# Kernel tuning notes

Measured on AMD Instinct MI355X. Metric: run time of the kernel, lower is better.

The kernel has to match this reference:

```python
import jax, jax.numpy as jnp
import numpy as np

B, S, E, H = 2, 2048, 1024, 16
D = E // H  # head_dim = 64
EPS = 1e-6


def _angle_decay():
    # angle: 1/10000**linspace(0,1,D//2), each value repeated twice (interleaved)
    a = 1.0 / (10000.0 ** jnp.linspace(0.0, 1.0, D // 2))
    angle = jnp.repeat(a, 2)  # [D]
    decay = jnp.log(1.0 - 2.0 ** (-5.0 - jnp.arange(H, dtype=jnp.float32)))  # [H]
    return angle, decay


def _rel_pos(slen):
    angle, decay = _angle_decay()
    idx = jnp.arange(slen, dtype=jnp.float32)
    sin = jnp.sin(idx[:, None] * angle[None, :])  # [S, D]
    cos = jnp.cos(idx[:, None] * angle[None, :])  # [S, D]
    diff = idx[:, None] - idx[None, :]            # [S, S]
    tril = diff >= 0
    masked = jnp.where(tril, diff, jnp.inf)
    mask = jnp.exp(masked * decay[:, None, None])  # [H, S, S]; exp(-inf)=0 on upper tri
    mask = jnp.nan_to_num(mask)
    mask = mask / jnp.sqrt(jnp.sum(mask, axis=-1, keepdims=True))
    return sin, cos, mask


def _rotate_every_two(x):
    x1 = x[..., ::2]
    x2 = x[..., 1::2]
    return jnp.stack((-x2, x1), axis=-1).reshape(x.shape)


def _theta_shift(x, sin, cos):
    # x: [B, H, S, D]; sin/cos: [S, D] broadcast over B,H
    return x * cos + _rotate_every_two(x) * sin


def setup_inputs() -> dict:
    key = jax.random.key(0)
    ks = jax.random.split(key, 5)
    scale = 1.0 / np.sqrt(E)
    return {
        "x": jax.random.normal(ks[0], (B, S, E), dtype=jnp.float32),
        "Wq": jax.random.normal(ks[1], (E, E), dtype=jnp.float32) * scale,
        "Wk": jax.random.normal(ks[2], (E, E), dtype=jnp.float32) * scale,
        "Wv": jax.random.normal(ks[3], (E, E), dtype=jnp.float32) * scale,
        "Wg": jax.random.normal(ks[4], (E, E), dtype=jnp.float32) * scale,
    }


def reference(x, Wq, Wk, Wv, Wg):
    bsz, tgt_len, _ = x.shape
    sin, cos, mask = _rel_pos(tgt_len)
    scaling = E ** (-0.5)

    q = x @ Wq
    k = (x @ Wk) * scaling
    v = x @ Wv
    g = x @ Wg

    q = q.reshape(bsz, tgt_len, H, D).transpose(0, 2, 1, 3)  # [B,H,S,D]
    k = k.reshape(bsz, tgt_len, H, D).transpose(0, 2, 1, 3)
    vr = v.reshape(bsz, tgt_len, H, D).transpose(0, 2, 1, 3)

    qr = _theta_shift(q, sin, cos)
    kr = _theta_shift(k, sin, cos)

    qk = jnp.einsum("bhqd,bhkd->bhqk", qr, kr) * mask[None]
    denom = jax.lax.stop_gradient(
        jnp.clip(jnp.sum(jnp.abs(qk), axis=-1, keepdims=True), 1.0, 5e4)
    )
    out = jnp.einsum("bhqk,bhkd->bhqd", qk / denom, vr)
    out = out.transpose(0, 2, 1, 3)  # [B,S,H,D]

    # RMSNorm over head_dim (no affine)
    out = out * jax.lax.rsqrt(jnp.mean(out * out, axis=-1, keepdims=True) + EPS)
    out = out.reshape(bsz, tgt_len, E)
    return jax.nn.silu(g) * out
```

## Files before the change

kernel.cpp:

```cpp
#include <hip/hip_runtime.h>

typedef unsigned short u16;
typedef unsigned int u32;
typedef __attribute__((ext_vector_type(8))) __bf16 bf16x8;
typedef __attribute__((ext_vector_type(4))) float f32x4;

#define B_SZ   2
#define S_LEN  2048
#define E_DIM  1024
#define NHEAD  16
#define HD     64
#define KDIM   1024

__device__ __forceinline__ float bf2f(u16 u){
  union { u32 i; float f; } c; c.i = ((u32)u) << 16; return c.f;
}
__device__ __forceinline__ u16 f2bf(float f){
  union { float f; u32 i; } c; c.f = f;
  return (u16)((c.i + 0x7FFFu + ((c.i >> 16) & 1u)) >> 16);
}
__device__ __forceinline__ u32 cvtpk_bf16(float lo, float hi){
  u32 r; asm("v_cvt_pk_bf16_f32 %0, %1, %2" : "=v"(r) : "v"(lo), "v"(hi)); return r;
}
__device__ __forceinline__ void gl2lds16(const void* g, void* l){
  __builtin_amdgcn_global_load_lds((const __attribute__((address_space(1))) void*)g,
                                   (__attribute__((address_space(3))) void*)l, 16, 0, 0);
}

__global__ __launch_bounds__(256) void prep_kernel(const float* __restrict__ x,
                                                   const float* __restrict__ Wq, const float* __restrict__ Wk,
                                                   const float* __restrict__ Wv, const float* __restrict__ Wg,
                                                   u16* __restrict__ xb, u16* __restrict__ WT){
  __shared__ u16 tile[64][66];
  int z = blockIdx.z;
  int t = threadIdx.x;
  if (z < 4){
    const float* Ws[4] = {Wq, Wk, Wv, Wg};
    const float* W = Ws[z];
    int n0 = blockIdx.x * 64, k0 = blockIdx.y * 64;
    int r = t >> 2, cg = (t & 3) * 16;
    const float* src = W + (size_t)(k0 + r) * E_DIM + n0 + cg;
    float f[16];
    #pragma unroll
    for (int c = 0; c < 4; c++) *(float4*)&f[c * 4] = *(const float4*)&src[c * 4];
    #pragma unroll
    for (int i = 0; i < 16; i++) tile[r][cg + i] = f2bf(f[i]);
    __syncthreads();
    u16 ov[16];
    #pragma unroll
    for (int i = 0; i < 16; i++) ov[i] = tile[cg + i][r];
    int n7 = r & 7, cb = cg >> 3;
    u16* dst = WT + (size_t)(z * E_DIM + n0 + r) * KDIM + k0;
    *(uint4*)&dst[(cb ^ n7) * 8]       = *(uint4*)&ov[0];
    *(uint4*)&dst[((cb + 1) ^ n7) * 8] = *(uint4*)&ov[8];
  } else {
    int blk = (z - 4) * 256 + blockIdx.y * 16 + blockIdx.x;
    size_t flat = ((size_t)blk * 256 + t) * 16;
    int m7 = (int)((flat >> 10) & 7);
    int cb = (int)((flat >> 3) & 7);
    size_t tl = flat & ~(size_t)63;
    float f[16];
    #pragma unroll
    for (int c = 0; c < 4; c++) *(float4*)&f[c * 4] = *(const float4*)&x[flat + c * 4];
    u16 o[16];
    #pragma unroll
    for (int i = 0; i < 16; i++) o[i] = f2bf(f[i]);
    *(uint4*)&xb[tl + ((cb ^ m7) * 8)]       = *(uint4*)&o[0];
    *(uint4*)&xb[tl + (((cb + 1) ^ m7) * 8)] = *(uint4*)&o[8];
  }
}

__global__ __launch_bounds__(512, 2) void gemm_kernel(const u16* __restrict__ A, const u16* __restrict__ Bt,
                                                      u16* __restrict__ qr, u16* __restrict__ kr,
                                                      u16* __restrict__ vt, u16* __restrict__ gc){
  __shared__ __align__(16) u16 SH[65536];
  int m0 = blockIdx.y * 256, n0 = blockIdx.x * 256;
  int t = threadIdx.x;
  int wave = t >> 6, lane = t & 63;
  int l15 = lane & 15, quad = lane >> 4, h8 = lane & 7;
  int wm = wave >> 2, wn = wave & 3;

  f32x4 acc[8][4];
  #pragma unroll
  for (int i = 0; i < 8; i++)
    #pragma unroll
    for (int j = 0; j < 4; j++) acc[i][j] = (f32x4){0.f, 0.f, 0.f, 0.f};

  auto Aoff = [&](int buf, int half) -> int { return (buf * 2 + half) * 8192; };
  auto Boff = [&](int buf, int half) -> int { return 32768 + (buf * 2 + half) * 8192; };

  auto stA = [&](int buf, int half, int kt){
    const u16* src = A + (size_t)(m0 + half * 128) * KDIM + kt * 64;
    #pragma unroll
    for (int c = 0; c < 2; c++){
      int L = c * 512 + t;
      gl2lds16(src + (size_t)(L >> 3) * KDIM + (L & 7) * 8, &SH[Aoff(buf, half) + L * 8]);
    }
  };
  auto stB = [&](int buf, int half, int kt){
    const u16* src = Bt + (size_t)(n0 + half * 128) * KDIM + kt * 64;
    #pragma unroll
    for (int c = 0; c < 2; c++){
      int L = c * 512 + t;
      gl2lds16(src + (size_t)(L >> 3) * KDIM + (L & 7) * 8, &SH[Boff(buf, half) + L * 8]);
    }
  };
  auto ldA = [&](int buf, int i, int ks) -> bf16x8 {
    int r = i * 16 + l15;
    return *(const bf16x8*)&SH[Aoff(buf, wm) + r * 64 + (((ks * 4 + quad) ^ h8) * 8)];
  };
  auto ldB = [&](int buf, int j, int ks) -> bf16x8 {
    int c = (wn & 1) * 64 + j * 16 + l15;
    return *(const bf16x8*)&SH[Boff(buf, wn >> 1) + c * 64 + (((ks * 4 + quad) ^ h8) * 8)];
  };

  stA(0, 0, 0); stB(0, 0, 0); stA(0, 1, 0); stB(0, 1, 0);
  asm volatile("s_waitcnt vmcnt(0)" ::: "memory");
  __builtin_amdgcn_s_barrier();

  bf16x8 a[4][2];
  bf16x8 bA[2][2];
  bf16x8 bB[2][2];

  for (int t2 = 0; t2 < 8; ++t2){
    int kt0 = 2 * t2;
    bool more = (t2 < 7);

    #pragma unroll
    for (int half = 0; half < 2; ++half){
      int buf = half;
      bool stg = (buf == 0) || more;
      {
        #pragma unroll
        for (int i = 0; i < 4; i++){ a[i][0] = ldA(buf, i, 0); a[i][1] = ldA(buf, i, 1); }
        #pragma unroll
        for (int j = 0; j < 2; j++){ bA[j][0] = ldB(buf, j, 0); bA[j][1] = ldB(buf, j, 1); }
        if (buf == 0){ stA(1, 0, kt0 + 1); stB(1, 0, kt0 + 1); }
        else if (more){ stA(0, 0, kt0 + 2); stB(0, 0, kt0 + 2); }
        __builtin_amdgcn_sched_barrier(0);
        __builtin_amdgcn_s_barrier();
        asm volatile("s_waitcnt lgkmcnt(0)" ::: "memory");
        __builtin_amdgcn_sched_barrier(0);
        __builtin_amdgcn_s_setprio(1);
        #pragma unroll
        for (int i = 0; i < 4; i++)
          #pragma unroll
          for (int j = 0; j < 2; j++){
            acc[i][j] = __builtin_amdgcn_mfma_f32_16x16x32_bf16(a[i][0], bA[j][0], acc[i][j], 0, 0, 0);
            acc[i][j] = __builtin_amdgcn_mfma_f32_16x16x32_bf16(a[i][1], bA[j][1], acc[i][j], 0, 0, 0);
          }
        __builtin_amdgcn_s_setprio(0);
        __builtin_amdgcn_sched_barrier(0);
        __builtin_amdgcn_s_barrier();
      }
      {
        #pragma unroll
        for (int j = 0; j < 2; j++){ bB[j][0] = ldB(buf, j + 2, 0); bB[j][1] = ldB(buf, j + 2, 1); }
        if (buf == 0){ stA(1, 1, kt0 + 1); stB(1, 1, kt0 + 1); }
        else if (more){ stA(0, 1, kt0 + 2); stB(0, 1, kt0 + 2); }
        __builtin_amdgcn_sched_barrier(0);
        __builtin_amdgcn_s_barrier();
        asm volatile("s_waitcnt lgkmcnt(0)" ::: "memory");
        __builtin_amdgcn_sched_barrier(0);
        __builtin_amdgcn_s_setprio(1);
        #pragma unroll
        for (int i = 0; i < 4; i++)
          #pragma unroll
          for (int j = 0; j < 2; j++){
            acc[i][j + 2] = __builtin_amdgcn_mfma_f32_16x16x32_bf16(a[i][0], bB[j][0], acc[i][j + 2], 0, 0, 0);
            acc[i][j + 2] = __builtin_amdgcn_mfma_f32_16x16x32_bf16(a[i][1], bB[j][1], acc[i][j + 2], 0, 0, 0);
          }
        __builtin_amdgcn_s_setprio(0);
        __builtin_amdgcn_sched_barrier(0);
        __builtin_amdgcn_s_barrier();
      }
      {
        #pragma unroll
        for (int i = 0; i < 4; i++){ a[i][0] = ldA(buf, i + 4, 0); a[i][1] = ldA(buf, i + 4, 1); }
        __builtin_amdgcn_sched_barrier(0);
        __builtin_amdgcn_s_barrier();
        asm volatile("s_waitcnt lgkmcnt(0)" ::: "memory");
        __builtin_amdgcn_sched_barrier(0);
        __builtin_amdgcn_s_setprio(1);
        #pragma unroll
        for (int i = 0; i < 4; i++)
          #pragma unroll
          for (int j = 0; j < 2; j++){
            acc[i + 4][j + 2] = __builtin_amdgcn_mfma_f32_16x16x32_bf16(a[i][0], bB[j][0], acc[i + 4][j + 2], 0, 0, 0);
            acc[i + 4][j + 2] = __builtin_amdgcn_mfma_f32_16x16x32_bf16(a[i][1], bB[j][1], acc[i + 4][j + 2], 0, 0, 0);
          }
        #pragma unroll
        for (int i = 0; i < 4; i++)
          #pragma unroll
          for (int j = 0; j < 2; j++){
            acc[i + 4][j] = __builtin_amdgcn_mfma_f32_16x16x32_bf16(a[i][0], bA[j][0], acc[i + 4][j], 0, 0, 0);
            acc[i + 4][j] = __builtin_amdgcn_mfma_f32_16x16x32_bf16(a[i][1], bA[j][1], acc[i + 4][j], 0, 0, 0);
          }
        __builtin_amdgcn_s_setprio(0);
        __builtin_amdgcn_sched_barrier(0);
        if (stg) { asm volatile("s_waitcnt vmcnt(0)" ::: "memory"); }
        __builtin_amdgcn_s_barrier();
      }
    }
  }

  __syncthreads();
  u16* epi = SH + wave * 8192;
  int zone = n0 >> 10;
  int n0l = n0 & 1023;
  int hh = (n0l >> 6) + wn;
  int b = m0 >> 11;
  int s0f = (m0 & 2047) + wm * 128;

  if (zone == 2){
    #pragma unroll
    for (int j = 0; j < 4; j++){
      int d = j * 16 + l15;
      #pragma unroll
      for (int i = 0; i < 8; i++){
        int cs0 = i * 2 + (quad >> 1);
        u16 pk[4];
        #pragma unroll
        for (int r = 0; r < 4; r++) pk[r] = f2bf(acc[i][j][r]);
        *(uint2*)&epi[d * 128 + ((cs0 ^ (d & 7)) * 8) + (quad & 1) * 4] = *(uint2*)pk;
      }
    }
    __syncthreads();
    int dl = lane >> 4, cl = lane & 15;
    size_t vbase = (size_t)((b << 4) + hh) * HD * S_LEN;
    #pragma unroll
    for (int it = 0; it < 16; it++){
      int d = it * 4 + dl;
      uint4 v = *(const uint4*)&epi[d * 128 + cl * 8];
      *(uint4*)&vt[vbase + (size_t)d * S_LEN + s0f + cl * 8] = v;
    }
  } else if (zone == 3){
    #pragma unroll
    for (int j = 0; j < 4; j++){
      int c0c = 2 * j + (l15 >> 3), o7 = l15 & 7;
      #pragma unroll
      for (int i = 0; i < 8; i++)
        #pragma unroll
        for (int r = 0; r < 4; r++){
          int row = i * 16 + quad * 4 + r;
          epi[row * 64 + ((c0c ^ (row & 7)) * 8) + o7] = f2bf(acc[i][j][r]);
        }
    }
    __syncthreads();
    int rl = lane >> 3, cl = lane & 7;
    #pragma unroll
    for (int it = 0; it < 16; it++){
      int row = it * 8 + rl;
      uint4 v = *(const uint4*)&epi[row * 64 + ((cl ^ (row & 7)) * 8)];
      *(uint4*)&gc[(size_t)(m0 + wm * 128 + row) * E_DIM + n0l + wn * 64 + cl * 8] = v;
    }
  } else {
    float scale = (zone == 1) ? 0.03125f : 1.0f;
    float sgn = (l15 & 1) ? 1.0f : -1.0f;
    #pragma unroll
    for (int j = 0; j < 4; j++){
      int d = j * 16 + l15;
      int c0c = 2 * j + (l15 >> 3), o7 = l15 & 7;
      float af = exp2f(-(float)(d >> 1) * (13.287712379549449f / 31.0f));
      float cs, sn, ca1, sa1, cb, sb_;
      __sincosf((float)(s0f + quad * 4) * af, &sn, &cs);
      __sincosf(af, &sa1, &ca1);
      __sincosf(13.0f * af, &sb_, &cb);
      #pragma unroll
      for (int i = 0; i < 8; i++)
        #pragma unroll
        for (int r = 0; r < 4; r++){
          int row = i * 16 + quad * 4 + r;
          float vv = acc[i][j][r] * scale;
          float p = __shfl_xor(vv, 1);
          float outv = vv * cs + sgn * p * sn;
          epi[row * 64 + ((c0c ^ (row & 7)) * 8) + o7] = f2bf(outv);
          float nc, ns;
          if (r < 3){ nc = cs * ca1 - sn * sa1; ns = sn * ca1 + cs * sa1; }
          else      { nc = cs * cb  - sn * sb_; ns = sn * cb  + cs * sb_; }
          cs = nc; sn = ns;
        }
    }
    __syncthreads();
    int rl = lane >> 3, cl = lane & 7;
    size_t qkbase = (size_t)((b << 4) + hh) * S_LEN + s0f;
    u16* dst = (zone == 0) ? qr : kr;
    #pragma unroll
    for (int it = 0; it < 16; it++){
      int row = it * 8 + rl;
      int rp = (zone == 0) ? (cl ^ (row & 7)) : cl;
      uint4 v = *(const uint4*)&epi[row * 64 + rp * 8];
      *(uint4*)&dst[(qkbase + row) * HD + cl * 8] = v;
    }
  }
}

__global__ __launch_bounds__(256, 3) void retention_kernel(const u16* __restrict__ qr, const u16* __restrict__ kr,
                                                           const u16* __restrict__ vt,
                                                           u16* __restrict__ pO, u16* __restrict__ pBa){
  __shared__ __align__(16) u16 Ks[2][4096];
  __shared__ __align__(16) u16 Vs[2][4096];
  __shared__ __align__(16) u16 Ps[128 * 72];
  int bh = blockIdx.x;
  int qb = 15 - (int)blockIdx.y;
  int z  = blockIdx.z;
  int h = bh & 15;
  int q0 = qb * 128;

  float decay = log1pf(-exp2f(-5.0f - (float)h));
  float negd = -decay;
  float win_f = 11.0f / negd;
  int win_i = (win_f > 2.1e9f) ? 0x7f000000 : (int)win_f;
  int nk = 2 * qb + 2;
  int z_lo = (z * nk) >> 2;
  int z_hi = (((z + 1) * nk) >> 2) - 1;
  int kb_lo = z_lo;
  {
    int jmin = q0 - win_i;
    if (jmin > z_lo * 64){ int wlo = jmin >> 6; kb_lo = wlo > z_lo ? wlo : z_lo; }
  }
  if (kb_lo > z_hi) return;

  int t = threadIdx.x, wave = t >> 6, lane = t & 63;
  int l15 = lane & 15, quad = lane >> 4, h8 = lane & 7;
  float estep = __expf(64.0f * negd);

  int qsE[2], rowb[2];
  #pragma unroll
  for (int e = 0; e < 2; e++){ rowb[e] = wave * 32 + e * 16; qsE[e] = q0 + rowb[e]; }

  bf16x8 qB[2][2];
  #pragma unroll
  for (int e = 0; e < 2; e++){
    size_t qrow = ((size_t)bh * S_LEN + qsE[e] + l15) * HD;
    qB[e][0] = *(const bf16x8*)&qr[qrow + quad * 8];
    qB[e][1] = *(const bf16x8*)&qr[qrow + 32 + quad * 8];
  }

  int k0s = kb_lo * 64;
  float em1d = expm1f(decay);
  float rfE[2]; int iE[2];
  #pragma unroll
  for (int e = 0; e < 2; e++){
    int i = qsE[e] + l15;
    iE[e] = i;
    float rowsum = expm1f((float)(i + 1) * decay) / em1d;
    rfE[e] = __expf((float)(i - k0s) * decay) * rsqrtf(rowsum);
  }
  float e1 = __expf(negd);
  float c16 = __expf(negd * 16.0f);
  float cbr[4];
  cbr[0] = __expf(negd * (float)(quad * 4));
  cbr[1] = cbr[0] * e1; cbr[2] = cbr[1] * e1; cbr[3] = cbr[2] * e1;

  f32x4 o[2][4];
  #pragma unroll
  for (int e = 0; e < 2; e++)
    #pragma unroll
    for (int dt = 0; dt < 4; dt++) o[e][dt] = (f32x4){0.f, 0.f, 0.f, 0.f};
  float babs[2] = {0.f, 0.f};

  const u16* krbh = kr + (size_t)bh * S_LEN * HD;
  const u16* vtbh = vt + (size_t)bh * HD * S_LEN;

  auto stKV = [&](int kb, int slot){
    int k0 = kb * 64;
    #pragma unroll
    for (int c = 0; c < 2; c++){
      int L = c * 256 + t;
      gl2lds16(krbh + (size_t)k0 * HD + L * 8, &Ks[slot][L * 8]);
    }
    #pragma unroll
    for (int c = 0; c < 2; c++){
      int L = c * 256 + t;
      gl2lds16(vtbh + (size_t)(L >> 3) * S_LEN + k0 + (L & 7) * 8, &Vs[slot][L * 8]);
    }
  };

  stKV(kb_lo, 0);
  __syncthreads();
  int cur = 0;
  for (int kb = kb_lo; kb <= z_hi; kb++){
    if (kb < z_hi) stKV(kb + 1, cur ^ 1);

    int k0 = kb * 64;
    const u16* KsC = &Ks[cur][0];
    const u16* VsC = &Vs[cur][0];

    bf16x8 kA0[4], kA1[4];
    #pragma unroll
    for (int ct = 0; ct < 4; ct++){
      int rw = (ct * 16 + l15) * 64;
      kA0[ct] = *(const bf16x8*)&KsC[rw + ((quad ^ h8) * 8)];
      kA1[ct] = *(const bf16x8*)&KsC[rw + (((quad + 4) ^ h8) * 8)];
    }
    #pragma unroll
    for (int e = 0; e < 2; e++){
      int qs = qsE[e];
      if (k0 <= qs + 15 && k0 + 63 >= qs - win_i){
        float rc0 = rfE[e] * cbr[0], rc1 = rfE[e] * cbr[1];
        float rc2 = rfE[e] * cbr[2], rc3 = rfE[e] * cbr[3];
        if (k0 + 64 <= qs){
          #pragma unroll
          for (int ct = 0; ct < 4; ct++){
            f32x4 zacc = (f32x4){0.f, 0.f, 0.f, 0.f};
            zacc = __builtin_amdgcn_mfma_f32_16x16x32_bf16(kA0[ct], qB[e][0], zacc, 0, 0, 0);
            zacc = __builtin_amdgcn_mfma_f32_16x16x32_bf16(kA1[ct], qB[e][1], zacc, 0, 0, 0);
            float p0 = zacc[0] * rc0, p1 = zacc[1] * rc1, p2 = zacc[2] * rc2, p3 = zacc[3] * rc3;
            babs[e] += fabsf(p0); babs[e] += fabsf(p1); babs[e] += fabsf(p2); babs[e] += fabsf(p3);
            u32 lo = cvtpk_bf16(p0, p1), hi = cvtpk_bf16(p2, p3);
            rc0 *= c16; rc1 *= c16; rc2 *= c16; rc3 *= c16;
            *(uint2*)&Ps[(rowb[e] + l15) * 72 + ct * 16 + quad * 4] = make_uint2(lo, hi);
          }
        } else {
          #pragma unroll
          for (int ct = 0; ct < 4; ct++){
            f32x4 zacc = (f32x4){0.f, 0.f, 0.f, 0.f};
            zacc = __builtin_amdgcn_mfma_f32_16x16x32_bf16(kA0[ct], qB[e][0], zacc, 0, 0, 0);
            zacc = __builtin_amdgcn_mfma_f32_16x16x32_bf16(kA1[ct], qB[e][1], zacc, 0, 0, 0);
            int kbase = k0 + ct * 16 + quad * 4;
            float p0 = zacc[0] * rc0, p1 = zacc[1] * rc1, p2 = zacc[2] * rc2, p3 = zacc[3] * rc3;
            if (kbase + 0 > iE[e]) p0 = 0.f;
            if (kbase + 1 > iE[e]) p1 = 0.f;
            if (kbase + 2 > iE[e]) p2 = 0.f;
            if (kbase + 3 > iE[e]) p3 = 0.f;
            babs[e] += fabsf(p0); babs[e] += fabsf(p1); babs[e] += fabsf(p2); babs[e] += fabsf(p3);
            u32 lo = cvtpk_bf16(p0, p1), hi = cvtpk_bf16(p2, p3);
            rc0 *= c16; rc1 *= c16; rc2 *= c16; rc3 *= c16;
            *(uint2*)&Ps[(rowb[e] + l15) * 72 + ct * 16 + quad * 4] = make_uint2(lo, hi);
          }
        }
      }
    }
    #pragma unroll
    for (int e = 0; e < 2; e++){
      int qs = qsE[e];
      if (k0 <= qs + 15 && k0 + 63 >= qs - win_i){
        bf16x8 pB0 = *(const bf16x8*)&Ps[(rowb[e] + l15) * 72 + quad * 8];
        bf16x8 pB1 = *(const bf16x8*)&Ps[(rowb[e] + l15) * 72 + 32 + quad * 8];
        #pragma unroll
        for (int dt = 0; dt < 4; dt++){
          int rw = (dt * 16 + l15) * 64;
          bf16x8 vA0 = *(const bf16x8*)&VsC[rw + ((quad ^ h8) * 8)];
          bf16x8 vA1 = *(const bf16x8*)&VsC[rw + (((quad + 4) ^ h8) * 8)];
          o[e][dt] = __builtin_amdgcn_mfma_f32_16x16x32_bf16(vA0, pB0, o[e][dt], 0, 0, 0);
          o[e][dt] = __builtin_amdgcn_mfma_f32_16x16x32_bf16(vA1, pB1, o[e][dt], 0, 0, 0);
        }
      }
    }
    #pragma unroll
    for (int e = 0; e < 2; e++) rfE[e] *= estep;
    __syncthreads();
    cur ^= 1;
  }

  size_t slot = ((size_t)bh * 16 + qb) * 4 + z;
  u16* po = pO + slot * (4 * 128 * 16);
  #pragma unroll
  for (int e = 0; e < 2; e++){
    float bsum = babs[e];
    bsum += __shfl_xor(bsum, 16);
    bsum += __shfl_xor(bsum, 32);
    if (quad == 0) pBa[slot * 128 + rowb[e] + l15] = f2bf(bsum);
    #pragma unroll
    for (int dt = 0; dt < 4; dt++){
      u16 pk[4];
      #pragma unroll
      for (int r = 0; r < 4; r++) pk[r] = f2bf(o[e][dt][r]);
      *(uint2*)&po[(dt * 128 + rowb[e] + l15) * 16 + quad * 4] = *(uint2*)pk;
    }
  }
}

__global__ __launch_bounds__(128) void combine_kernel(const u16* __restrict__ pO, const u16* __restrict__ pBa,
                                                      const u16* __restrict__ gc, float* __restrict__ out){
  int bh = blockIdx.x, qb = blockIdx.y;
  int b = bh >> 4, h = bh & 15;
  int i = threadIdx.x;
  int s = qb * 128 + i;
  size_t s4 = ((size_t)bh * 16 + qb) * 4;

  float decay = log1pf(-exp2f(-5.0f - (float)h));
  float negd = -decay;
  float win_f = 11.0f / negd;
  int win_i = (win_f > 2.1e9f) ? 0x7f000000 : (int)win_f;
  int nk = 2 * qb + 2;
  int q0 = qb * 128;

  float v[64];
  #pragma unroll
  for (int d = 0; d < 64; d++) v[d] = 0.f;
  float bsum = 0.f;
  #pragma unroll
  for (int z = 0; z < 4; z++){
    int z_lo = (z * nk) >> 2;
    int z_hi = (((z + 1) * nk) >> 2) - 1;
    int kb_lo = z_lo;
    {
      int jmin = q0 - win_i;
      if (jmin > z_lo * 64){ int wlo = jmin >> 6; kb_lo = wlo > z_lo ? wlo : z_lo; }
    }
    if (kb_lo > z_hi) continue;
    const u16* pz = pO + (s4 + z) * 8192;
    #pragma unroll
    for (int dt = 0; dt < 4; dt++){
      u16 a[16];
      *(uint4*)&a[0] = *(const uint4*)&pz[(dt * 128 + i) * 16];
      *(uint4*)&a[8] = *(const uint4*)&pz[(dt * 128 + i) * 16 + 8];
      #pragma unroll
      for (int c = 0; c < 16; c++) v[dt * 16 + c] += bf2f(a[c]);
    }
    bsum += bf2f(pBa[(s4 + z) * 128 + i]);
  }
  float dinv = 1.0f / fminf(fmaxf(bsum, 1.0f), 50000.0f);
  float ssq = 0.f;
  #pragma unroll
  for (int d = 0; d < 64; d++){ v[d] *= dinv; ssq += v[d] * v[d]; }
  float rms = rsqrtf(ssq * (1.0f / 64.0f) + 1e-6f);
  size_t gbase = ((size_t)b * S_LEN + s) * E_DIM + h * HD;
  u16 gu[64];
  #pragma unroll
  for (int c = 0; c < 8; c++) *(uint4*)&gu[c * 8] = *(const uint4*)&gc[gbase + c * 8];
  float ov[64];
  #pragma unroll
  for (int d = 0; d < 64; d++){
    float gv = bf2f(gu[d]);
    float sg = gv / (1.0f + __expf(-gv));
    ov[d] = v[d] * rms * sg;
  }
  float* obase = out + ((size_t)b * S_LEN + s) * E_DIM + h * HD;
  #pragma unroll
  for (int c = 0; c < 16; c++) *(float4*)&obase[c * 4] = *(float4*)&ov[c * 4];
}

extern "C" void kernel_launch(void* const* d_in, const int* in_sizes, int n_in,
                              void* d_out, int out_size, void* d_ws, size_t ws_size,
                              hipStream_t stream){
  const float* x  = (const float*)d_in[0];
  const float* Wq = (const float*)d_in[1];
  const float* Wk = (const float*)d_in[2];
  const float* Wv = (const float*)d_in[3];
  const float* Wg = (const float*)d_in[4];
  float* out = (float*)d_out;
  char* ws = (char*)d_ws;
  u16* xb  = (u16*)(ws);
  u16* WT  = (u16*)(ws + (8ull  << 20));
  u16* pO  = (u16*)(ws);
  u16* qrp = (u16*)(ws + (32ull << 20));
  u16* krp = (u16*)(ws + (40ull << 20));
  u16* vtp = (u16*)(ws + (48ull << 20));
  u16* gcp = (u16*)(ws + (56ull << 20));
  u16* pBa = (u16*)(ws + (64ull << 20));

  prep_kernel     <<<dim3(16, 16, 8),  256, 0, stream>>>(x, Wq, Wk, Wv, Wg, xb, WT);
  gemm_kernel     <<<dim3(16, 16),     512, 0, stream>>>(xb, WT, qrp, krp, vtp, gcp);
  retention_kernel<<<dim3(32, 16, 4),  256, 0, stream>>>(qrp, krp, vtp, pO, pBa);
  combine_kernel  <<<dim3(32, 16),     128, 0, stream>>>(pO, pBa, gcp, out);
}
```

Before: 170.7 us.

## Drop split-K partitioning and fuse combine epilogue into retention kernel

Removes the 4-way key-range split of the retention kernel, so each block walks the full causal/windowed key range for its 128 query rows. The normalization, RMSNorm and SiLU gating epilogue is moved into the retention kernel, which deletes the combine kernel and the bf16 partial-output round trip through global memory. The trade-off is fewer blocks (512 instead of up to 2048) with longer, unbalanced per-block work for late query blocks, which may reduce parallelism and load balance. The fused epilogue writes fp32 output with 16-byte stores scattered across the MFMA lane layout.

```diff
diff --git a/kernel.cpp b/kernel.cpp
--- a/kernel.cpp
+++ b/kernel.cpp
@@ -297,29 +297,25 @@
 
 __global__ __launch_bounds__(256, 3) void retention_kernel(const u16* __restrict__ qr, const u16* __restrict__ kr,
                                                            const u16* __restrict__ vt,
-                                                           u16* __restrict__ pO, u16* __restrict__ pBa){
+                                                           const u16* __restrict__ gc, float* __restrict__ out){
   __shared__ __align__(16) u16 Ks[2][4096];
   __shared__ __align__(16) u16 Vs[2][4096];
   __shared__ __align__(16) u16 Ps[128 * 72];
   int bh = blockIdx.x;
   int qb = 15 - (int)blockIdx.y;
-  int z  = blockIdx.z;
-  int h = bh & 15;
+  int h = bh & 15, b = bh >> 4;
   int q0 = qb * 128;
 
   float decay = log1pf(-exp2f(-5.0f - (float)h));
   float negd = -decay;
   float win_f = 11.0f / negd;
   int win_i = (win_f > 2.1e9f) ? 0x7f000000 : (int)win_f;
-  int nk = 2 * qb + 2;
-  int z_lo = (z * nk) >> 2;
-  int z_hi = (((z + 1) * nk) >> 2) - 1;
-  int kb_lo = z_lo;
+  int z_hi = 2 * qb + 1;
+  int kb_lo = 0;
   {
     int jmin = q0 - win_i;
-    if (jmin > z_lo * 64){ int wlo = jmin >> 6; kb_lo = wlo > z_lo ? wlo : z_lo; }
-  }
-  if (kb_lo > z_hi) return;
+    if (jmin > 0) kb_lo = jmin >> 6;
+  }
 
   int t = threadIdx.x, wave = t >> 6, lane = t & 63;
   int l15 = lane & 15, quad = lane >> 4, h8 = lane & 7;
@@ -454,83 +450,43 @@
     cur ^= 1;
   }
 
-  size_t slot = ((size_t)bh * 16 + qb) * 4 + z;
-  u16* po = pO + slot * (4 * 128 * 16);
   #pragma unroll
   for (int e = 0; e < 2; e++){
     float bsum = babs[e];
     bsum += __shfl_xor(bsum, 16);
     bsum += __shfl_xor(bsum, 32);
-    if (quad == 0) pBa[slot * 128 + rowb[e] + l15] = f2bf(bsum);
+    float dinv = 1.0f / fminf(fmaxf(bsum, 1.0f), 50000.0f);
+    float vv[4][4];
+    float ssq = 0.f;
+    #pragma unroll
+    for (int dt = 0; dt < 4; dt++)
+      #pragma unroll
+      for (int r = 0; r < 4; r++){
+        float v = o[e][dt][r] * dinv;
+        vv[dt][r] = v;
+        ssq += v * v;
+      }
+    ssq += __shfl_xor(ssq, 16);
+    ssq += __shfl_xor(ssq, 32);
+    float rms = rsqrtf(ssq * (1.0f / 64.0f) + 1e-6f);
+    int row = qsE[e] + l15;
+    size_t base = ((size_t)b * S_LEN + row) * E_DIM + h * HD;
     #pragma unroll
     for (int dt = 0; dt < 4; dt++){
-      u16 pk[4];
+      int d0 = dt * 16 + quad * 4;
+      uint2 g2 = *(const uint2*)&gc[base + d0];
+      u16 ga[4];
+      *(uint2*)ga = g2;
+      float ov[4];
       #pragma unroll
-      for (int r = 0; r < 4; r++) pk[r] = f2bf(o[e][dt][r]);
-      *(uint2*)&po[(dt * 128 + rowb[e] + l15) * 16 + quad * 4] = *(uint2*)pk;
-    }
-  }
-}
-
-__global__ __launch_bounds__(128) void combine_kernel(const u16* __restrict__ pO, const u16* __restrict__ pBa,
-                                                      const u16* __restrict__ gc, float* __restrict__ out){
-  int bh = blockIdx.x, qb = blockIdx.y;
-  int b = bh >> 4, h = bh & 15;
-  int i = threadIdx.x;
-  int s = qb * 128 + i;
-  size_t s4 = ((size_t)bh * 16 + qb) * 4;
-
-  float decay = log1pf(-exp2f(-5.0f - (float)h));
-  float negd = -decay;
-  float win_f = 11.0f / negd;
-  int win_i = (win_f > 2.1e9f) ? 0x7f000000 : (int)win_f;
-  int nk = 2 * qb + 2;
-  int q0 = qb * 128;
-
-  float v[64];
-  #pragma unroll
-  for (int d = 0; d < 64; d++) v[d] = 0.f;
-  float bsum = 0.f;
-  #pragma unroll
-  for (int z = 0; z < 4; z++){
-    int z_lo = (z * nk) >> 2;
-    int z_hi = (((z + 1) * nk) >> 2) - 1;
-    int kb_lo = z_lo;
-    {
-      int jmin = q0 - win_i;
-      if (jmin > z_lo * 64){ int wlo = jmin >> 6; kb_lo = wlo > z_lo ? wlo : z_lo; }
-    }
-    if (kb_lo > z_hi) continue;
-    const u16* pz = pO + (s4 + z) * 8192;
-    #pragma unroll
-    for (int dt = 0; dt < 4; dt++){
-      u16 a[16];
-      *(uint4*)&a[0] = *(const uint4*)&pz[(dt * 128 + i) * 16];
-      *(uint4*)&a[8] = *(const uint4*)&pz[(dt * 128 + i) * 16 + 8];
-      #pragma unroll
-      for (int c = 0; c < 16; c++) v[dt * 16 + c] += bf2f(a[c]);
-    }
-    bsum += bf2f(pBa[(s4 + z) * 128 + i]);
-  }
-  float dinv = 1.0f / fminf(fmaxf(bsum, 1.0f), 50000.0f);
-  float ssq = 0.f;
-  #pragma unroll
-  for (int d = 0; d < 64; d++){ v[d] *= dinv; ssq += v[d] * v[d]; }
-  float rms = rsqrtf(ssq * (1.0f / 64.0f) + 1e-6f);
-  size_t gbase = ((size_t)b * S_LEN + s) * E_DIM + h * HD;
-  u16 gu[64];
-  #pragma unroll
-  for (int c = 0; c < 8; c++) *(uint4*)&gu[c * 8] = *(const uint4*)&gc[gbase + c * 8];
-  float ov[64];
-  #pragma unroll
-  for (int d = 0; d < 64; d++){
-    float gv = bf2f(gu[d]);
-    float sg = gv / (1.0f + __expf(-gv));
-    ov[d] = v[d] * rms * sg;
-  }
-  float* obase = out + ((size_t)b * S_LEN + s) * E_DIM + h * HD;
-  #pragma unroll
-  for (int c = 0; c < 16; c++) *(float4*)&obase[c * 4] = *(float4*)&ov[c * 4];
+      for (int r = 0; r < 4; r++){
+        float gv = bf2f(ga[r]);
+        float sg = gv / (1.0f + __expf(-gv));
+        ov[r] = vv[dt][r] * rms * sg;
+      }
+      *(float4*)&out[base + d0] = *(float4*)ov;
+    }
+  }
 }
 
 extern "C" void kernel_launch(void* const* d_in, const int* in_sizes, int n_in,
@@ -545,15 +501,12 @@
   char* ws = (char*)d_ws;
   u16* xb  = (u16*)(ws);
   u16* WT  = (u16*)(ws + (8ull  << 20));
-  u16* pO  = (u16*)(ws);
   u16* qrp = (u16*)(ws + (32ull << 20));
   u16* krp = (u16*)(ws + (40ull << 20));
   u16* vtp = (u16*)(ws + (48ull << 20));
   u16* gcp = (u16*)(ws + (56ull << 20));
-  u16* pBa = (u16*)(ws + (64ull << 20));
 
   prep_kernel     <<<dim3(16, 16, 8),  256, 0, stream>>>(x, Wq, Wk, Wv, Wg, xb, WT);
   gemm_kernel     <<<dim3(16, 16),     512, 0, stream>>>(xb, WT, qrp, krp, vtp, gcp);
-  retention_kernel<<<dim3(32, 16, 4),  256, 0, stream>>>(qrp, krp, vtp, pO, pBa);
-  combine_kernel  <<<dim3(32, 16),     128, 0, stream>>>(pO, pBa, gcp, out);
-}
+  retention_kernel<<<dim3(32, 16),     256, 0, stream>>>(qrp, krp, vtp, gcp, out);
+}
```

After: 170.9 us. About the same (+0.1%).
